# Kernel optimization log

Hardware: AMD Instinct MI355X
Metric: run time of the kernel (lower is better)

## Reference

```python
import jax, jax.numpy as jnp
import numpy as np
from jax.ops import segment_sum, segment_max

B, P, NP, EP = 128, 16, 256, 1280
EPG, ODIM, NH = 2048, 256, 128
EPS = 1e-5


def _bn(x, g, b):
    # BatchNorm1d (training-mode batch statistics), biased variance like torch
    mu = x.mean(0)
    var = ((x - mu) ** 2).mean(0)
    return g * (x - mu) * jax.lax.rsqrt(var + EPS) + b


def _gat(feat, src, dst, W, al, ar, resW, bias):
    # DGL GATConv: fc -> per-head attn logits -> leaky_relu -> edge softmax over dst -> aggregate; + residual fc + bias
    n = feat.shape[0]
    H, D = al.shape
    z = (feat @ W).reshape(n, H, D)
    el = (z * al).sum(-1)                                  # [n,H]
    er = (z * ar).sum(-1)
    e = jax.nn.leaky_relu(el[src] + er[dst], 0.2)          # [E,H]
    m = segment_max(e, dst, num_segments=n)
    ex = jnp.exp(e - m[dst])
    s = segment_sum(ex, dst, num_segments=n)
    a = ex / (s[dst] + 1e-9)
    rst = segment_sum(a[:, :, None] * z[src], dst, num_segments=n)  # [n,H,D]
    res = (feat @ resW).reshape(n, H, D)
    return (rst + res + bias.reshape(1, H, D)).reshape(n, H * D)


def _plane(feat, src, dst, p):
    # PlaneGraphEncoder forward (eval: dropout off)
    h = _gat(feat, src, dst, p['W1'], p['al1'], p['ar1'], p['res1'], p['b1'])
    h = jax.nn.relu(_bn(h, p['g1'], p['be1']))
    h = _gat(h, src, dst, p['W2'], p['al2'], p['ar2'], p['res2'], p['b2'])
    h = jax.nn.relu(_bn(h, p['g2'], p['be2']))
    rep = h.mean(0)                                        # dgl.mean_nodes -> [32]
    d = jax.nn.relu(_bn(h @ p['dW1'] + p['db1'], p['dg'], p['dbe']))
    recon = d @ p['dW2'] + p['db2']                        # [n,1]
    rloss = jnp.mean((recon - feat) ** 2)
    return rep, rloss


def _masked_gc(h, src, dst, mask_f, W, b):
    # DGL GraphConv(norm='both') with edge_weight = mask[src]*mask[dst]; structural degrees, clamp>=1
    n = h.shape[0]
    ones = jnp.ones(src.shape[0], h.dtype)
    d_out = jnp.maximum(segment_sum(ones, src, num_segments=n), 1.0)
    d_in = jnp.maximum(segment_sum(ones, dst, num_segments=n), 1.0)
    ew = mask_f[src] * mask_f[dst]                         # [E]
    hs = h * jax.lax.rsqrt(d_out)[:, None]
    agg = segment_sum(ew[:, None] * hs[src], dst, num_segments=n)
    return (agg * jax.lax.rsqrt(d_in)[:, None]) @ W + b


def _forward(plane_feat, original_features,
             W1, al1, ar1, res1, b1, g1, be1,
             W2, al2, ar2, res2, b2, g2, be2,
             dW1, db1, dg, dbe, dW2, db2,
             ft_W, ft_b, ft_g, ft_be, gc_W, gc_b, gbn_g, gbn_be,
             c1_W, c1_b, ln_g, ln_be, c2_W, c2_b,
             plane_src, plane_dst, patient_src, patient_dst, mask):
    pp = dict(W1=W1, al1=al1, ar1=ar1, res1=res1, b1=b1, g1=g1, be1=be1,
              W2=W2, al2=al2, ar2=ar2, res2=res2, b2=b2, g2=g2, be2=be2,
              dW1=dW1, db1=db1, dg=dg, dbe=dbe, dW2=dW2, db2=db2)
    enc_b = jax.vmap(_plane, in_axes=(0, 0, 0, None))      # over patients
    enc_pb = jax.vmap(enc_b, in_axes=(1, 1, 1, 0))         # over planes (params axis 0)
    reps, rlosses = enc_pb(plane_feat, plane_src, plane_dst, pp)   # [P,B,32], [P,B]
    plane_rep = jnp.transpose(reps, (1, 0, 2)).reshape(plane_feat.shape[0], -1)  # [B, P*32]
    avg_recon = rlosses.mean()                             # sum / (B*P)

    x = jnp.concatenate([original_features, plane_rep], axis=1)   # [B, fused]
    h = jax.nn.relu(_bn(x @ ft_W + ft_b, ft_g, ft_be))
    mask_f = mask.astype(h.dtype)
    h_sum = h
    for i in range(3):
        hn = _masked_gc(h, patient_src, patient_dst, mask_f, gc_W[i], gc_b[i])
        hn = jax.nn.relu(_bn(hn, gbn_g[i], gbn_be[i]))
        h = hn + h
        h_sum = h_sum + h
    h = h_sum / 4.0                                        # mean over [h0,h1,h2,h3]

    z = h @ c1_W + c1_b
    mu = z.mean(-1, keepdims=True)
    var = ((z - mu) ** 2).mean(-1, keepdims=True)
    z = jax.nn.relu(ln_g * (z - mu) * jax.lax.rsqrt(var + EPS) + ln_be)
    logits = z @ c2_W + c2_b
    return logits, avg_recon


def setup_inputs() -> dict:
    key = jax.random.key(0)
    ks = iter(jax.random.split(key, 64))
    f = lambda shape, s=0.1: jax.random.normal(next(ks), shape, jnp.float32) * s
    inp = dict(
        plane_feat=f((B, P, NP, 1), 1.0),
        plane_src=jax.random.randint(next(ks), (B, P, EP), 0, NP, jnp.int32),
        plane_dst=jax.random.randint(next(ks), (B, P, EP), 0, NP, jnp.int32),
        patient_src=jax.random.randint(next(ks), (EPG,), 0, B, jnp.int32),
        patient_dst=jax.random.randint(next(ks), (EPG,), 0, B, jnp.int32),
        original_features=f((B, ODIM), 1.0),
        mask=jax.random.randint(next(ks), (B,), 0, 2, jnp.int32),
        # per-plane encoder params, stacked over P
        W1=f((P, 1, 128)), al1=f((P, 2, 64)), ar1=f((P, 2, 64)),
        res1=f((P, 1, 128)), b1=f((P, 128)),
        g1=jnp.ones((P, 128)), be1=jnp.zeros((P, 128)),
        W2=f((P, 128, 32)), al2=f((P, 1, 32)), ar2=f((P, 1, 32)),
        res2=f((P, 128, 32)), b2=f((P, 32)),
        g2=jnp.ones((P, 32)), be2=jnp.zeros((P, 32)),
        dW1=f((P, 32, 128)), db1=f((P, 128)),
        dg=jnp.ones((P, 128)), dbe=jnp.zeros((P, 128)),
        dW2=f((P, 128, 1)), db2=f((P, 1)),
        # patient-level params
        ft_W=f((ODIM + P * 32, NH)), ft_b=f((NH,)),
        ft_g=jnp.ones((NH,)), ft_be=jnp.zeros((NH,)),
        gc_W=f((3, NH, NH)), gc_b=f((3, NH)),
        gbn_g=jnp.ones((3, NH)), gbn_be=jnp.zeros((3, NH)),
        c1_W=f((NH, NH // 2)), c1_b=f((NH // 2,)),
        ln_g=jnp.ones((NH // 2,)), ln_be=jnp.zeros((NH // 2,)),
        c2_W=f((NH // 2, 2)), c2_b=f((2,)),
    )
    return inp


def reference(plane_feat, plane_src, plane_dst, patient_src, patient_dst,
              original_features, mask,
              W1, al1, ar1, res1, b1, g1, be1,
              W2, al2, ar2, res2, b2, g2, be2,
              dW1, db1, dg, dbe, dW2, db2,
              ft_W, ft_b, ft_g, ft_be, gc_W, gc_b, gbn_g, gbn_be,
              c1_W, c1_b, ln_g, ln_be, c2_W, c2_b):
    return _forward(plane_feat, original_features,
                    W1, al1, ar1, res1, b1, g1, be1,
                    W2, al2, ar2, res2, b2, g2, be2,
                    dW1, db1, dg, dbe, dW2, db2,
                    ft_W, ft_b, ft_g, ft_be, gc_W, gc_b, gbn_g, gbn_be,
                    c1_W, c1_b, ln_g, ln_be, c2_W, c2_b,
                    plane_src, plane_dst, patient_src, patient_dst, mask)
```

## Files before the change

### kernel.cpp

```cpp
#include <hip/hip_runtime.h>

#define B_    128
#define P_    16
#define NP_   256
#define EP_   1280
#define EPG_  2048
#define ODIM_ 256
#define NH_   128

typedef __attribute__((ext_vector_type(8))) short s8_t;
typedef __attribute__((ext_vector_type(4))) short s4_t;
typedef __attribute__((ext_vector_type(4))) float f4_t;

__device__ __forceinline__ unsigned short f2b(float x) {
  unsigned u = __builtin_bit_cast(unsigned, x);
  u = (u + 0x7fffu + ((u >> 16) & 1u)) >> 16;
  return (unsigned short)u;
}
__device__ __forceinline__ float b2f(short x) {
  unsigned u = ((unsigned)(unsigned short)x) << 16;
  return __builtin_bit_cast(float, u);
}

struct SmemA {
  float f[256];
  union {
    __align__(16) unsigned short wT1[64 * 136];
    __align__(16) unsigned short z2[256 * 40];
  } u1;
  __align__(16) unsigned short dW1T[128 * 36];
  union {
    struct { float S0a[256]; float S1a[256]; } a;
    float redf[512];
  } u2;
  float el2[256], er2[256];
  union {
    struct { float abg0[128], abg1[128], abg2[128]; } a;
    struct { float al2v[32], ar2v[32], dW2v[128]; } b;
  } u3;
  union {
    int cnt[256];
    struct { float scA[32], shA[32], dscA[64], dshA[64]; } b;
  } u4;
  unsigned short esrc[1280];
  int wtot[4];
  float r8[4][8]; float stat[8]; float wA[2], wB[2];
  float rlacc;
};

__global__ __launch_bounds__(256, 3) void plane_enc(
    const float* __restrict__ feat, const int* __restrict__ esrcg, const int* __restrict__ edstg,
    const float* __restrict__ W1, const float* __restrict__ al1, const float* __restrict__ ar1,
    const float* __restrict__ res1, const float* __restrict__ b1, const float* __restrict__ g1,
    const float* __restrict__ be1,
    const float* __restrict__ W2, const float* __restrict__ al2, const float* __restrict__ ar2,
    const float* __restrict__ res2, const float* __restrict__ g2, const float* __restrict__ be2,
    const float* __restrict__ dW1, const float* __restrict__ dg, const float* __restrict__ dbe,
    const float* __restrict__ dW2, const float* __restrict__ db2,
    float* __restrict__ rep_out, float* __restrict__ rlp_out)
{
  __shared__ SmemA s;
  const int g = blockIdx.x;
  const int p = g & 15;
  const int t = threadIdx.x;
  const int lane = t & 63, wv = t >> 6;
  const int l15 = lane & 15, quad = lane >> 4;

  s.f[t] = feat[g * NP_ + t];
  if (t == 0) s.rlacc = 0.f;
  s.u4.cnt[t] = 0;
  __syncthreads();

  const int* gs = esrcg + g * EP_;
  const int* gd = edstg + g * EP_;
  for (int k = t; k < EP_; k += 256) atomicAdd(&s.u4.cnt[gd[k]], 1);
  __syncthreads();
  int v = s.u4.cnt[t];
  int incl = v;
  #pragma unroll
  for (int off = 1; off < 64; off <<= 1) {
    int n = __shfl_up(incl, off, 64);
    if (lane >= off) incl += n;
  }
  if (lane == 63) s.wtot[wv] = incl;
  __syncthreads();
  int woff = 0;
  for (int w = 0; w < wv; w++) woff += s.wtot[w];
  const int myStart = woff + incl - v;
  const int myDeg = v;
  __syncthreads();
  s.u4.cnt[t] = myStart;
  __syncthreads();
  for (int k = t; k < EP_; k += 256) {
    int d = gd[k];
    int pos = atomicAdd(&s.u4.cnt[d], 1);
    s.esrc[pos] = (unsigned short)gs[k];
  }
  {
    const float* W2g = W2 + p * 4096;
    const float* Rg  = res2 + p * 4096;
    for (int q = 0; q < 16; q++) {
      int idx = t + 256 * q;
      int k = idx >> 5, n = idx & 31;
      s.u1.wT1[n * 136 + k]        = f2b(W2g[idx]);
      s.u1.wT1[(n + 32) * 136 + k] = f2b(Rg[idx]);
    }
  }
  if (t < 128) {
    float w1v = W1[p * 128 + t];
    float a  = w1v * al1[p * 128 + t];
    float bq = w1v * ar1[p * 128 + t];
    #pragma unroll
    for (int off = 32; off > 0; off >>= 1) {
      a  += __shfl_down(a, off, 64);
      bq += __shfl_down(bq, off, 64);
    }
    if (lane == 0) { s.wA[wv] = a; s.wB[wv] = bq; }
  }
  __syncthreads();

  const float fi = s.f[t];
  float S0, S1;
  {
    const float wa0 = s.wA[0], wb0 = s.wB[0], wa1 = s.wA[1], wb1 = s.wB[1];
    float fmx = -1e30f, fmn = 1e30f;
    for (int j = 0; j < myDeg; j++) {
      float fs = s.f[s.esrc[myStart + j]];
      fmx = fmaxf(fmx, fs); fmn = fminf(fmn, fs);
    }
    float x0s = (wa0 >= 0.f) ? fmx : fmn;
    float x1s = (wa1 >= 0.f) ? fmx : fmn;
    float m0 = wa0 * x0s + wb0 * fi; m0 = m0 > 0.f ? m0 : 0.2f * m0;
    float m1 = wa1 * x1s + wb1 * fi; m1 = m1 > 0.f ? m1 : 0.2f * m1;
    float ss0 = 0.f, ss1 = 0.f, U0 = 0.f, U1 = 0.f;
    for (int j = 0; j < myDeg; j++) {
      float fs = s.f[s.esrc[myStart + j]];
      float e0 = wa0 * fs + wb0 * fi; e0 = e0 > 0.f ? e0 : 0.2f * e0;
      float e1 = wa1 * fs + wb1 * fi; e1 = e1 > 0.f ? e1 : 0.2f * e1;
      float x0 = __expf(e0 - m0), x1 = __expf(e1 - m1);
      ss0 += x0; U0 += x0 * fs;
      ss1 += x1; U1 += x1 * fs;
    }
    S0 = U0 / (ss0 + 1e-9f);
    S1 = U1 / (ss1 + 1e-9f);
    s.u2.a.S0a[t] = S0; s.u2.a.S1a[t] = S1;
  }

  {
    float vals[8] = {fi, fi * fi, S0, S0 * S0, S0 * fi, S1, S1 * S1, S1 * fi};
    #pragma unroll
    for (int d2 = 32; d2 > 0; d2 >>= 1) {
      #pragma unroll
      for (int q = 0; q < 8; q++) vals[q] += __shfl_down(vals[q], d2, 64);
    }
    if (lane == 0) {
      #pragma unroll
      for (int q = 0; q < 8; q++) s.r8[wv][q] = vals[q];
    }
  }
  __syncthreads();
  if (t < 8) s.stat[t] = (s.r8[0][t] + s.r8[1][t] + s.r8[2][t] + s.r8[3][t]) * (1.f / 256.f);
  __syncthreads();
  if (t < 128) {
    float mf = s.stat[0], ef2 = s.stat[1];
    int hh = t >> 6;
    float mS = s.stat[2 + 3 * hh], eS2 = s.stat[3 + 3 * hh], eSf = s.stat[4 + 3 * hh];
    float varS = eS2 - mS * mS, varf = ef2 - mf * mf, cov = eSf - mS * mf;
    float Wv = W1[p * 128 + t], Rv = res1[p * 128 + t], Bv = b1[p * 128 + t];
    float mu  = Wv * mS + Rv * mf + Bv;
    float var = Wv * Wv * varS + Rv * Rv * varf + 2.f * Wv * Rv * cov;
    float gn  = g1[p * 128 + t] * rsqrtf(var + 1e-5f);
    s.u3.a.abg0[t] = gn * Wv;
    s.u3.a.abg1[t] = gn * Rv;
    s.u3.a.abg2[t] = gn * (Bv - mu) + be1[p * 128 + t];
  }
  __syncthreads();

  float resv[32];
  {
    f4_t accum[4][4];
    #pragma unroll
    for (int i = 0; i < 4; i++)
      #pragma unroll
      for (int nt = 0; nt < 4; nt++) accum[i][nt] = (f4_t){0.f, 0.f, 0.f, 0.f};

    float fm[4], s0m[4], s1m[4];
    #pragma unroll
    for (int i = 0; i < 4; i++) {
      int m = (wv * 4 + i) * 16 + l15;
      fm[i] = s.f[m]; s0m[i] = s.u2.a.S0a[m]; s1m[i] = s.u2.a.S1a[m];
    }
    #pragma unroll
    for (int kt = 0; kt < 4; kt++) {
      int cbase = kt * 32 + quad * 8;
      float a0[8], a1[8], a2[8];
      #pragma unroll
      for (int j = 0; j < 8; j++) {
        a0[j] = s.u3.a.abg0[cbase + j]; a1[j] = s.u3.a.abg1[cbase + j]; a2[j] = s.u3.a.abg2[cbase + j];
      }
      s8_t afr[4];
      #pragma unroll
      for (int i = 0; i < 4; i++) {
        float Sm = (kt < 2) ? s0m[i] : s1m[i];
        union { s8_t v; unsigned short u[8]; } fu;
        #pragma unroll
        for (int j = 0; j < 8; j++) {
          float h = fmaxf(fmaf(a0[j], Sm, fmaf(a1[j], fm[i], a2[j])), 0.f);
          fu.u[j] = f2b(h);
        }
        afr[i] = fu.v;
      }
      s8_t bfr[4];
      #pragma unroll
      for (int nt = 0; nt < 4; nt++)
        bfr[nt] = *(const s8_t*)&s.u1.wT1[(nt * 16 + l15) * 136 + cbase];
      #pragma unroll
      for (int i = 0; i < 4; i++)
        #pragma unroll
        for (int nt = 0; nt < 4; nt++)
          accum[i][nt] = __builtin_amdgcn_mfma_f32_16x16x32_bf16(afr[i], bfr[nt], accum[i][nt], 0, 0, 0);
    }
    __syncthreads();
    #pragma unroll
    for (int i = 0; i < 4; i++) {
      int mBase = (wv * 4 + i) * 16 + quad * 4;
      #pragma unroll
      for (int nt = 0; nt < 2; nt++) {
        int col = nt * 16 + l15;
        #pragma unroll
        for (int r = 0; r < 4; r++)
          s.u1.z2[(mBase + r) * 40 + col] = f2b(accum[i][nt][r]);
      }
      #pragma unroll
      for (int h2 = 0; h2 < 2; h2++)
        #pragma unroll
        for (int r = 0; r < 4; r++)
          resv[(i * 2 + h2) * 4 + r] = accum[i][2 + h2][r];
    }
  }
  if (t < 32) { s.u3.b.al2v[t] = al2[p * 32 + t]; s.u3.b.ar2v[t] = ar2[p * 32 + t]; }
  if (t < 128) s.u3.b.dW2v[t] = dW2[p * 128 + t];
  {
    const float* Dg = dW1 + p * 4096;
    #pragma unroll
    for (int q = 0; q < 16; q++) {
      int idx = t + 256 * q;
      int k = idx >> 7, n = idx & 127;
      s.dW1T[n * 36 + k] = f2b(Dg[idx]);
    }
  }
  const float db2v = db2[p];
  __syncthreads();

  {
    const s8_t* zr = (const s8_t*)&s.u1.z2[t * 40];
    float el = 0.f, er = 0.f;
    #pragma unroll
    for (int q = 0; q < 4; q++) {
      s8_t vz = zr[q];
      #pragma unroll
      for (int j = 0; j < 8; j++) {
        float zv = b2f(vz[j]);
        el += zv * s.u3.b.al2v[q * 8 + j];
        er += zv * s.u3.b.ar2v[q * 8 + j];
      }
    }
    s.el2[t] = el; s.er2[t] = er;
  }
  __syncthreads();

  float hrow[32];
  {
    const float eri = s.er2[t];
    float maxel = -1e30f;
    for (int j = 0; j < myDeg; j++)
      maxel = fmaxf(maxel, s.el2[s.esrc[myStart + j]]);
    float m = maxel + eri; m = m > 0.f ? m : 0.2f * m;
    float ss = 0.f;
    #pragma unroll
    for (int d2 = 0; d2 < 32; d2++) hrow[d2] = 0.f;
    for (int j = 0; j < myDeg; j++) {
      int sj = s.esrc[myStart + j];
      float e = s.el2[sj] + eri;
      e = e > 0.f ? e : 0.2f * e;
      float x = __expf(e - m);
      ss += x;
      const s8_t* zr = (const s8_t*)&s.u1.z2[sj * 40];
      #pragma unroll
      for (int q = 0; q < 4; q++) {
        s8_t vz = zr[q];
        #pragma unroll
        for (int jj = 0; jj < 8; jj++) hrow[q * 8 + jj] += x * b2f(vz[jj]);
      }
    }
    float inv = 1.f / (ss + 1e-9f);
    #pragma unroll
    for (int d2 = 0; d2 < 32; d2++) hrow[d2] *= inv;
  }
  __syncthreads();
  #pragma unroll
  for (int i = 0; i < 4; i++) {
    int mBase = (wv * 4 + i) * 16 + quad * 4;
    #pragma unroll
    for (int h2 = 0; h2 < 2; h2++) {
      int col = h2 * 16 + l15;
      #pragma unroll
      for (int r = 0; r < 4; r++)
        s.u1.z2[(mBase + r) * 40 + col] = f2b(resv[(i * 2 + h2) * 4 + r]);
    }
  }
  __syncthreads();
  {
    const s8_t* zr = (const s8_t*)&s.u1.z2[t * 40];
    #pragma unroll
    for (int q = 0; q < 4; q++) {
      s8_t vz = zr[q];
      #pragma unroll
      for (int jj = 0; jj < 8; jj++) hrow[q * 8 + jj] += b2f(vz[jj]);
    }
  }
  #pragma unroll
  for (int d2 = 0; d2 < 32; d2++) s.u1.z2[t * 40 + d2] = f2b(hrow[d2]);
  __syncthreads();

  {
    int c = t & 31, gq = t >> 5;
    float s1 = 0.f, s2 = 0.f;
    for (int j = 0; j < 32; j++) {
      float vz = b2f((short)s.u1.z2[(gq * 32 + j) * 40 + c]);
      s1 += vz; s2 += vz * vz;
    }
    s.u2.redf[t] = s1; s.u2.redf[256 + t] = s2;
  }
  __syncthreads();
  if (t < 32) {
    float s1 = 0.f, s2 = 0.f;
    #pragma unroll
    for (int q = 0; q < 8; q++) { s1 += s.u2.redf[q * 32 + t]; s2 += s.u2.redf[256 + q * 32 + t]; }
    float mu = s1 * (1.f / 256.f);
    float var = s2 * (1.f / 256.f) - mu * mu;
    float a = g2[p * 32 + t] * rsqrtf(var + 1e-5f);
    s.u4.b.scA[t] = a; s.u4.b.shA[t] = be2[p * 32 + t] - a * mu;
  }
  __syncthreads();
  {
    int c = t & 31, gq = t >> 5;
    float a = s.u4.b.scA[c], bb = s.u4.b.shA[c];
    float s1 = 0.f;
    for (int j = 0; j < 32; j++) {
      int ad = (gq * 32 + j) * 40 + c;
      float vz = b2f((short)s.u1.z2[ad]);
      float hv = fmaxf(a * vz + bb, 0.f);
      s.u1.z2[ad] = f2b(hv);
      s1 += hv;
    }
    s.u2.redf[t] = s1;
  }
  __syncthreads();
  if (t < 32) {
    float s1 = 0.f;
    #pragma unroll
    for (int q = 0; q < 8; q++) s1 += s.u2.redf[q * 32 + t];
    rep_out[g * 32 + t] = s1 * (1.f / 256.f);
  }
  __syncthreads();

  {
    s8_t afr2[4];
    #pragma unroll
    for (int i = 0; i < 4; i++)
      afr2[i] = *(const s8_t*)&s.u1.z2[((wv * 4 + i) * 16 + l15) * 40 + quad * 8];
    float rAcc[4][4];
    #pragma unroll
    for (int i = 0; i < 4; i++)
      #pragma unroll
      for (int r = 0; r < 4; r++) rAcc[i][r] = 0.f;

    for (int half = 0; half < 2; half++) {
      __syncthreads();
      s.u2.redf[t] = 0.f; s.u2.redf[256 + t] = 0.f;
      __syncthreads();
      f4_t acc2[4][4];
      #pragma unroll
      for (int i = 0; i < 4; i++)
        #pragma unroll
        for (int nt = 0; nt < 4; nt++) acc2[i][nt] = (f4_t){0.f, 0.f, 0.f, 0.f};
      s8_t bfr[4];
      #pragma unroll
      for (int nt = 0; nt < 4; nt++) {
        const s4_t* pr = (const s4_t*)&s.dW1T[(half * 64 + nt * 16 + l15) * 36 + quad * 8];
        s4_t lo = pr[0], hi = pr[1];
        bfr[nt] = __builtin_shufflevector(lo, hi, 0, 1, 2, 3, 4, 5, 6, 7);
      }
      #pragma unroll
      for (int i = 0; i < 4; i++)
        #pragma unroll
        for (int nt = 0; nt < 4; nt++)
          acc2[i][nt] = __builtin_amdgcn_mfma_f32_16x16x32_bf16(afr2[i], bfr[nt], acc2[i][nt], 0, 0, 0);
      #pragma unroll
      for (int nt = 0; nt < 4; nt++) {
        float s1 = 0.f, s2 = 0.f;
        #pragma unroll
        for (int i = 0; i < 4; i++)
          #pragma unroll
          for (int r = 0; r < 4; r++) { float vv = acc2[i][nt][r]; s1 += vv; s2 += vv * vv; }
        atomicAdd(&s.u2.redf[nt * 16 + l15], s1);
        atomicAdd(&s.u2.redf[256 + nt * 16 + l15], s2);
      }
      __syncthreads();
      if (t < 64) {
        int col = half * 64 + t;
        float mu = s.u2.redf[t] * (1.f / 256.f);
        float var = s.u2.redf[256 + t] * (1.f / 256.f) - mu * mu;
        float a = dg[p * 128 + col] * rsqrtf(var + 1e-5f);
        s.u4.b.dscA[t] = a; s.u4.b.dshA[t] = dbe[p * 128 + col] - a * mu;
      }
      __syncthreads();
      #pragma unroll
      for (int nt = 0; nt < 4; nt++) {
        int cl = nt * 16 + l15;
        float a = s.u4.b.dscA[cl], bb = s.u4.b.dshA[cl], w2 = s.u3.b.dW2v[half * 64 + cl];
        #pragma unroll
        for (int i = 0; i < 4; i++)
          #pragma unroll
          for (int r = 0; r < 4; r++) {
            float dv = fmaxf(a * acc2[i][nt][r] + bb, 0.f);
            rAcc[i][r] += dv * w2;
          }
      }
    }
    #pragma unroll
    for (int off = 1; off < 16; off <<= 1)
      #pragma unroll
      for (int i = 0; i < 4; i++)
        #pragma unroll
        for (int r = 0; r < 4; r++) rAcc[i][r] += __shfl_xor(rAcc[i][r], off, 64);
    if (l15 == 0) {
      float sq = 0.f;
      #pragma unroll
      for (int i = 0; i < 4; i++)
        #pragma unroll
        for (int r = 0; r < 4; r++) {
          int m = (wv * 4 + i) * 16 + quad * 4 + r;
          float diff = rAcc[i][r] + db2v - s.f[m];
          sq += diff * diff;
        }
      atomicAdd(&s.rlacc, sq);
    }
  }
  __syncthreads();
  if (t == 0) rlp_out[g] = s.rlacc;
}

__global__ __launch_bounds__(256) void ft_mm(
    const float* __restrict__ orig, const float* __restrict__ rep,
    const float* __restrict__ ftW, float* __restrict__ hpre,
    const int* __restrict__ ps, const int* __restrict__ pd,
    const int* __restrict__ mask, unsigned short* __restrict__ abar,
    const float* __restrict__ gcW, unsigned short* __restrict__ gws)
{
  const int t = threadIdx.x;

  if (blockIdx.x >= 9) {
    const int layer = blockIdx.x - 9;
    const float* src = gcW + layer * 16384;
    unsigned short* dst = gws + layer * 16384;
    for (int idx = t; idx < 16384; idx += 256) dst[idx] = f2b(src[idx]);
    return;
  }

  if (blockIdx.x == 8) {
    __shared__ int aB[128 * 128];
    __shared__ int co[128], ci[128];
    __shared__ float facs[128], facd[128];
    for (int idx = t; idx < 16384; idx += 256) aB[idx] = 0;
    if (t < 128) { co[t] = 0; ci[t] = 0; }
    __syncthreads();
    for (int e = t; e < EPG_; e += 256) {
      int sN = ps[e], d = pd[e];
      atomicAdd(&co[sN], 1);
      atomicAdd(&ci[d], 1);
      atomicAdd(&aB[d * 128 + sN], 1);
    }
    __syncthreads();
    if (t < 128) {
      float mk = (float)mask[t];
      int da = co[t] > 1 ? co[t] : 1;
      int db = ci[t] > 1 ? ci[t] : 1;
      facs[t] = mk * rsqrtf((float)da);
      facd[t] = mk * rsqrtf((float)db);
    }
    __syncthreads();
    for (int idx = t; idx < 16384; idx += 256) {
      int d = idx >> 7, sN = idx & 127;
      abar[idx] = f2b((float)aB[idx] * facd[d] * facs[sN]);
    }
    return;
  }

  const int wv = t >> 6, lane = t & 63;
  const int l15 = lane & 15, quad = lane >> 4;
  const int m = blockIdx.x * 16 + l15;

  f4_t acc[2];
  acc[0] = (f4_t){0.f, 0.f, 0.f, 0.f};
  acc[1] = (f4_t){0.f, 0.f, 0.f, 0.f};
  for (int kt = 0; kt < 24; kt++) {
    int k0 = kt * 32 + quad * 8;
    const float* px = (k0 < 256) ? (orig + m * 256 + k0) : (rep + m * 512 + (k0 - 256));
    float4 xa = ((const float4*)px)[0];
    float4 xb = ((const float4*)px)[1];
    union { s8_t v; unsigned short u[8]; } fu;
    fu.u[0] = f2b(xa.x); fu.u[1] = f2b(xa.y); fu.u[2] = f2b(xa.z); fu.u[3] = f2b(xa.w);
    fu.u[4] = f2b(xb.x); fu.u[5] = f2b(xb.y); fu.u[6] = f2b(xb.z); fu.u[7] = f2b(xb.w);
    #pragma unroll
    for (int nt = 0; nt < 2; nt++) {
      int col = wv * 32 + nt * 16 + l15;
      union { s8_t v; unsigned short u[8]; } bu;
      #pragma unroll
      for (int j = 0; j < 8; j++) bu.u[j] = f2b(ftW[(k0 + j) * 128 + col]);
      acc[nt] = __builtin_amdgcn_mfma_f32_16x16x32_bf16(fu.v, bu.v, acc[nt], 0, 0, 0);
    }
  }
  #pragma unroll
  for (int nt = 0; nt < 2; nt++) {
    int col = wv * 32 + nt * 16 + l15;
    #pragma unroll
    for (int r = 0; r < 4; r++)
      hpre[(blockIdx.x * 16 + quad * 4 + r) * 128 + col] = acc[nt][r];
  }
}

struct SmemB {
  __align__(16) unsigned short arow[128 * 136];
  __align__(16) unsigned short hT[128 * 136];
  union {
    struct {
      union {
        __align__(16) unsigned short wT[128 * 136];
        float zF[128 * 68];
      } w;
      __align__(16) unsigned short aggB[128 * 136];
    } mm;
  } u;
  float redA[1024], redB[1024];
  float scB[128], shB[128];
};

__global__ __launch_bounds__(1024) void k_patient(
    const float* __restrict__ hpre, const unsigned short* __restrict__ abar,
    const float* __restrict__ ftg, const float* __restrict__ ftbe,
    const unsigned short* __restrict__ gws, const float* __restrict__ gbng,
    const float* __restrict__ gbnbe,
    const float* __restrict__ c1W, const float* __restrict__ c1b,
    const float* __restrict__ lng, const float* __restrict__ lnbe,
    const float* __restrict__ c2W, const float* __restrict__ c2b,
    const float* __restrict__ rlp, float* __restrict__ out)
{
  __shared__ SmemB s;
  const int t = threadIdx.x;
  const int w = t >> 6, lane = t & 63;
  const int l15 = lane & 15, quad = lane >> 4;
  const int mb = w & 7, nb = (w >> 3) * 64;

  for (int idx = t; idx < 16384; idx += 1024) {
    int d = idx >> 7, sN = idx & 127;
    s.arow[d * 136 + sN] = abar[idx];
  }

  f4_t acc[4];
  #pragma unroll
  for (int nt = 0; nt < 4; nt++) {
    int col = nb + nt * 16 + l15;
    #pragma unroll
    for (int r = 0; r < 4; r++)
      acc[nt][r] = hpre[(mb * 16 + quad * 4 + r) * 128 + col];
  }

  float hR[16], hsumR[16];
  {
    #pragma unroll
    for (int nt = 0; nt < 4; nt++) {
      float s1 = acc[nt][0] + acc[nt][1] + acc[nt][2] + acc[nt][3];
      float s2 = acc[nt][0]*acc[nt][0] + acc[nt][1]*acc[nt][1] + acc[nt][2]*acc[nt][2] + acc[nt][3]*acc[nt][3];
      s1 += __shfl_xor(s1, 16, 64); s1 += __shfl_xor(s1, 32, 64);
      s2 += __shfl_xor(s2, 16, 64); s2 += __shfl_xor(s2, 32, 64);
      if (quad == 0) {
        s.redA[mb * 128 + nb + nt * 16 + l15] = s1;
        s.redB[mb * 128 + nb + nt * 16 + l15] = s2;
      }
    }
    __syncthreads();
    if (t < 128) {
      float a1 = 0.f, a2 = 0.f;
      #pragma unroll
      for (int q = 0; q < 8; q++) { a1 += s.redA[q * 128 + t]; a2 += s.redB[q * 128 + t]; }
      float mu = a1 * (1.f / 128.f), var = a2 * (1.f / 128.f) - mu * mu;
      float a = ftg[t] * rsqrtf(var + 1e-5f);
      s.scB[t] = a; s.shB[t] = ftbe[t] - a * mu;
    }
    __syncthreads();
    #pragma unroll
    for (int nt = 0; nt < 4; nt++) {
      int col = nb + nt * 16 + l15;
      float a = s.scB[col], bb = s.shB[col];
      #pragma unroll
      for (int r = 0; r < 4; r++) {
        int row = mb * 16 + quad * 4 + r;
        float hv = fmaxf(a * acc[nt][r] + bb, 0.f);
        hR[nt * 4 + r] = hv; hsumR[nt * 4 + r] = hv;
        s.hT[col * 136 + row] = f2b(hv);
      }
    }
  }
  __syncthreads();

  for (int layer = 0; layer < 3; layer++) {
    #pragma unroll
    for (int q = 0; q < 16; q++) {
      int idx = t + 1024 * q;
      int kk = idx >> 7, n = idx & 127;
      s.u.mm.w.wT[n * 136 + kk] = gws[layer * 16384 + idx];
    }
    f4_t ag[4];
    #pragma unroll
    for (int nt = 0; nt < 4; nt++) ag[nt] = (f4_t){0.f, 0.f, 0.f, 0.f};
    #pragma unroll
    for (int ks = 0; ks < 4; ks++) {
      s8_t afr = *(const s8_t*)&s.arow[(mb * 16 + l15) * 136 + ks * 32 + quad * 8];
      #pragma unroll
      for (int nt = 0; nt < 4; nt++) {
        s8_t bfr = *(const s8_t*)&s.hT[(nb + nt * 16 + l15) * 136 + ks * 32 + quad * 8];
        ag[nt] = __builtin_amdgcn_mfma_f32_16x16x32_bf16(afr, bfr, ag[nt], 0, 0, 0);
      }
    }
    #pragma unroll
    for (int nt = 0; nt < 4; nt++) {
      int col = nb + nt * 16 + l15;
      #pragma unroll
      for (int r = 0; r < 4; r++)
        s.u.mm.aggB[(mb * 16 + quad * 4 + r) * 136 + col] = f2b(ag[nt][r]);
    }
    __syncthreads();
    f4_t oc[4];
    #pragma unroll
    for (int nt = 0; nt < 4; nt++) oc[nt] = (f4_t){0.f, 0.f, 0.f, 0.f};
    #pragma unroll
    for (int ks = 0; ks < 4; ks++) {
      s8_t afr = *(const s8_t*)&s.u.mm.aggB[(mb * 16 + l15) * 136 + ks * 32 + quad * 8];
      #pragma unroll
      for (int nt = 0; nt < 4; nt++) {
        s8_t bfr = *(const s8_t*)&s.u.mm.w.wT[(nb + nt * 16 + l15) * 136 + ks * 32 + quad * 8];
        oc[nt] = __builtin_amdgcn_mfma_f32_16x16x32_bf16(afr, bfr, oc[nt], 0, 0, 0);
      }
    }
    #pragma unroll
    for (int nt = 0; nt < 4; nt++) {
      float s1 = oc[nt][0] + oc[nt][1] + oc[nt][2] + oc[nt][3];
      float s2 = oc[nt][0]*oc[nt][0] + oc[nt][1]*oc[nt][1] + oc[nt][2]*oc[nt][2] + oc[nt][3]*oc[nt][3];
      s1 += __shfl_xor(s1, 16, 64); s1 += __shfl_xor(s1, 32, 64);
      s2 += __shfl_xor(s2, 16, 64); s2 += __shfl_xor(s2, 32, 64);
      if (quad == 0) {
        s.redA[mb * 128 + nb + nt * 16 + l15] = s1;
        s.redB[mb * 128 + nb + nt * 16 + l15] = s2;
      }
    }
    __syncthreads();
    if (t < 128) {
      float a1 = 0.f, a2 = 0.f;
      #pragma unroll
      for (int q = 0; q < 8; q++) { a1 += s.redA[q * 128 + t]; a2 += s.redB[q * 128 + t]; }
      float mu = a1 * (1.f / 128.f), var = a2 * (1.f / 128.f) - mu * mu;
      float a = gbng[layer * 128 + t] * rsqrtf(var + 1e-5f);
      s.scB[t] = a; s.shB[t] = gbnbe[layer * 128 + t] - a * mu;
    }
    __syncthreads();
    #pragma unroll
    for (int nt = 0; nt < 4; nt++) {
      int col = nb + nt * 16 + l15;
      float a = s.scB[col], bb = s.shB[col];
      #pragma unroll
      for (int r = 0; r < 4; r++) {
        int row = mb * 16 + quad * 4 + r;
        float hn = fmaxf(a * oc[nt][r] + bb, 0.f) + hR[nt * 4 + r];
        hR[nt * 4 + r] = hn;
        hsumR[nt * 4 + r] += hn;
        s.hT[col * 136 + row] = f2b(hn);
      }
    }
    __syncthreads();
  }

  #pragma unroll
  for (int nt = 0; nt < 4; nt++) {
    int col = nb + nt * 16 + l15;
    #pragma unroll
    for (int r = 0; r < 4; r++)
      s.u.mm.aggB[(mb * 16 + quad * 4 + r) * 136 + col] = f2b(hsumR[nt * 4 + r] * 0.25f);
  }
  #pragma unroll
  for (int q = 0; q < 8; q++) {
    int idx = t + 1024 * q;
    int n = idx & 63, kk = idx >> 6;
    s.u.mm.w.wT[n * 136 + kk] = f2b(c1W[kk * 64 + n]);
  }
  __syncthreads();
  {
    const int nb2 = (w >> 3) * 32;
    f4_t zc[2];
    #pragma unroll
    for (int nt = 0; nt < 2; nt++) zc[nt] = (f4_t){0.f, 0.f, 0.f, 0.f};
    #pragma unroll
    for (int ks = 0; ks < 4; ks++) {
      s8_t afr = *(const s8_t*)&s.u.mm.aggB[(mb * 16 + l15) * 136 + ks * 32 + quad * 8];
      #pragma unroll
      for (int nt = 0; nt < 2; nt++) {
        s8_t bfr = *(const s8_t*)&s.u.mm.w.wT[(nb2 + nt * 16 + l15) * 136 + ks * 32 + quad * 8];
        zc[nt] = __builtin_amdgcn_mfma_f32_16x16x32_bf16(afr, bfr, zc[nt], 0, 0, 0);
      }
    }
    __syncthreads();
    #pragma unroll
    for (int nt = 0; nt < 2; nt++) {
      int col = nb2 + nt * 16 + l15;
      #pragma unroll
      for (int r = 0; r < 4; r++)
        s.u.mm.w.zF[(mb * 16 + quad * 4 + r) * 68 + col] = zc[nt][r] + c1b[col];
    }
  }
  __syncthreads();
  if (t < 128) {
    float s1 = 0.f, s2 = 0.f;
    #pragma unroll
    for (int j = 0; j < 64; j++) { float zv = s.u.mm.w.zF[t * 68 + j]; s1 += zv; s2 += zv * zv; }
    float mu = s1 * (1.f / 64.f);
    float var = s2 * (1.f / 64.f) - mu * mu;
    float rs = rsqrtf(var + 1e-5f);
    float l0 = 0.f, l1 = 0.f;
    #pragma unroll
    for (int j = 0; j < 64; j++) {
      float zv = s.u.mm.w.zF[t * 68 + j];
      float zn = fmaxf(lng[j] * (zv - mu) * rs + lnbe[j], 0.f);
      l0 += zn * c2W[j * 2];
      l1 += zn * c2W[j * 2 + 1];
    }
    out[t * 2]     = l0 + c2b[0];
    out[t * 2 + 1] = l1 + c2b[1];
  }

  {
    float r = rlp[t] + rlp[t + 1024];
    #pragma unroll
    for (int off = 32; off > 0; off >>= 1) r += __shfl_down(r, off, 64);
    if (lane == 0) s.redA[w] = r;
  }
  __syncthreads();
  if (t == 0) {
    float tot = 0.f;
    #pragma unroll
    for (int i = 0; i < 16; i++) tot += s.redA[i];
    out[256] = tot * (1.f / (256.f * 2048.f));
  }
}

extern "C" void kernel_launch(void* const* d_in, const int* in_sizes, int n_in,
                              void* d_out, int out_size, void* d_ws, size_t ws_size,
                              hipStream_t stream) {
  (void)in_sizes; (void)n_in; (void)out_size; (void)ws_size;
  const float* plane_feat  = (const float*)d_in[0];
  const int*   plane_src   = (const int*)d_in[1];
  const int*   plane_dst   = (const int*)d_in[2];
  const int*   patient_src = (const int*)d_in[3];
  const int*   patient_dst = (const int*)d_in[4];
  const float* orig        = (const float*)d_in[5];
  const int*   mask        = (const int*)d_in[6];
  const float* W1   = (const float*)d_in[7];
  const float* al1  = (const float*)d_in[8];
  const float* ar1  = (const float*)d_in[9];
  const float* res1 = (const float*)d_in[10];
  const float* b1   = (const float*)d_in[11];
  const float* g1   = (const float*)d_in[12];
  const float* be1  = (const float*)d_in[13];
  const float* W2   = (const float*)d_in[14];
  const float* al2  = (const float*)d_in[15];
  const float* ar2  = (const float*)d_in[16];
  const float* res2 = (const float*)d_in[17];
  const float* g2   = (const float*)d_in[19];
  const float* be2  = (const float*)d_in[20];
  const float* dW1  = (const float*)d_in[21];
  const float* dg   = (const float*)d_in[23];
  const float* dbe  = (const float*)d_in[24];
  const float* dW2  = (const float*)d_in[25];
  const float* db2  = (const float*)d_in[26];
  const float* ftW  = (const float*)d_in[27];
  const float* ftg  = (const float*)d_in[29];
  const float* ftbe = (const float*)d_in[30];
  const float* gcW  = (const float*)d_in[31];
  const float* gbng = (const float*)d_in[33];
  const float* gbnbe= (const float*)d_in[34];
  const float* c1W  = (const float*)d_in[35];
  const float* c1b  = (const float*)d_in[36];
  const float* lng  = (const float*)d_in[37];
  const float* lnbe = (const float*)d_in[38];
  const float* c2W  = (const float*)d_in[39];
  const float* c2b  = (const float*)d_in[40];

  float* ws   = (float*)d_ws;
  float* rep  = ws;
  float* hpre = ws + 65536;
  unsigned short* abar = (unsigned short*)(ws + 81920);
  float* rlp  = ws + 90112;
  unsigned short* gws = (unsigned short*)(ws + 94208);
  float* outp = (float*)d_out;

  plane_enc<<<2048, 256, 0, stream>>>(plane_feat, plane_src, plane_dst,
      W1, al1, ar1, res1, b1, g1, be1, W2, al2, ar2, res2, g2, be2,
      dW1, dg, dbe, dW2, db2, rep, rlp);
  ft_mm<<<12, 256, 0, stream>>>(orig, rep, ftW, hpre,
      patient_src, patient_dst, mask, abar, gcW, gws);
  k_patient<<<1, 1024, 0, stream>>>(hpre, abar, ftg, ftbe,
      gws, gbng, gbnbe, c1W, c1b, lng, lnbe, c2W, c2b, rlp, outp);
}
```

Before: 316.5 us.

## Sort nodes by in-degree so wavefronts process similar-degree nodes together

Builds a per-graph degree histogram (capped at 32) and a counting-sort permutation of the nodes, then has each thread handle a degree-sorted node in both GAT aggregation loops. This targets wavefront divergence, where one high-degree node made all 64 lanes wait on the longest per-node edge loop. In exchange it adds shared-memory atomics, a serial prefix scan on thread 0, extra barriers, and scattered reads and writes through the permutation.

```diff
diff --git a/kernel.cpp b/kernel.cpp
--- a/kernel.cpp
+++ b/kernel.cpp
@@ -43,6 +43,8 @@
     struct { float scA[32], shA[32], dscA[64], dshA[64]; } b;
   } u4;
   unsigned short esrc[1280];
+  unsigned short mst[256], mdg[256], srt[256];
+  int hist[33];
   int wtot[4];
   float r8[4][8]; float stat[8]; float wA[2], wB[2];
   float rlacc;
@@ -90,7 +92,14 @@
   const int myDeg = v;
   __syncthreads();
   s.u4.cnt[t] = myStart;
-  __syncthreads();
+  s.mst[t] = (unsigned short)myStart;
+  s.mdg[t] = (unsigned short)myDeg;
+  if (t < 33) s.hist[t] = 0;
+  __syncthreads();
+  {
+    int b = myDeg < 32 ? myDeg : 32;
+    atomicAdd(&s.hist[b], 1);
+  }
   for (int k = t; k < EP_; k += 256) {
     int d = gd[k];
     int pos = atomicAdd(&s.u4.cnt[d], 1);
@@ -118,34 +127,48 @@
     if (lane == 0) { s.wA[wv] = a; s.wB[wv] = bq; }
   }
   __syncthreads();
-
-  const float fi = s.f[t];
-  float S0, S1;
-  {
+  if (t == 0) {
+    int acc = 0;
+    for (int i = 0; i < 33; i++) { int c = s.hist[i]; s.hist[i] = acc; acc += c; }
+  }
+  __syncthreads();
+  {
+    int b = myDeg < 32 ? myDeg : 32;
+    int pos = atomicAdd(&s.hist[b], 1);
+    s.srt[pos] = (unsigned short)t;
+  }
+  __syncthreads();
+
+  {
+    const int nid = s.srt[t];
+    const float fin = s.f[nid];
+    const int st2 = s.mst[nid], dg2 = s.mdg[nid];
     const float wa0 = s.wA[0], wb0 = s.wB[0], wa1 = s.wA[1], wb1 = s.wB[1];
     float fmx = -1e30f, fmn = 1e30f;
-    for (int j = 0; j < myDeg; j++) {
-      float fs = s.f[s.esrc[myStart + j]];
+    for (int j = 0; j < dg2; j++) {
+      float fs = s.f[s.esrc[st2 + j]];
       fmx = fmaxf(fmx, fs); fmn = fminf(fmn, fs);
     }
     float x0s = (wa0 >= 0.f) ? fmx : fmn;
     float x1s = (wa1 >= 0.f) ? fmx : fmn;
-    float m0 = wa0 * x0s + wb0 * fi; m0 = m0 > 0.f ? m0 : 0.2f * m0;
-    float m1 = wa1 * x1s + wb1 * fi; m1 = m1 > 0.f ? m1 : 0.2f * m1;
+    float m0 = wa0 * x0s + wb0 * fin; m0 = m0 > 0.f ? m0 : 0.2f * m0;
+    float m1 = wa1 * x1s + wb1 * fin; m1 = m1 > 0.f ? m1 : 0.2f * m1;
     float ss0 = 0.f, ss1 = 0.f, U0 = 0.f, U1 = 0.f;
-    for (int j = 0; j < myDeg; j++) {
-      float fs = s.f[s.esrc[myStart + j]];
-      float e0 = wa0 * fs + wb0 * fi; e0 = e0 > 0.f ? e0 : 0.2f * e0;
-      float e1 = wa1 * fs + wb1 * fi; e1 = e1 > 0.f ? e1 : 0.2f * e1;
+    for (int j = 0; j < dg2; j++) {
+      float fs = s.f[s.esrc[st2 + j]];
+      float e0 = wa0 * fs + wb0 * fin; e0 = e0 > 0.f ? e0 : 0.2f * e0;
+      float e1 = wa1 * fs + wb1 * fin; e1 = e1 > 0.f ? e1 : 0.2f * e1;
       float x0 = __expf(e0 - m0), x1 = __expf(e1 - m1);
       ss0 += x0; U0 += x0 * fs;
       ss1 += x1; U1 += x1 * fs;
     }
-    S0 = U0 / (ss0 + 1e-9f);
-    S1 = U1 / (ss1 + 1e-9f);
-    s.u2.a.S0a[t] = S0; s.u2.a.S1a[t] = S1;
-  }
-
+    s.u2.a.S0a[nid] = U0 / (ss0 + 1e-9f);
+    s.u2.a.S1a[nid] = U1 / (ss1 + 1e-9f);
+  }
+  __syncthreads();
+
+  const float fi = s.f[t];
+  const float S0 = s.u2.a.S0a[t], S1 = s.u2.a.S1a[t];
   {
     float vals[8] = {fi, fi * fi, S0, S0 * S0, S0 * fi, S1, S1 * S1, S1 * fi};
     #pragma unroll
@@ -270,17 +293,21 @@
   __syncthreads();
 
   float hrow[32];
-  {
-    const float eri = s.er2[t];
+  int nid2;
+  {
+    const int nid = s.srt[t];
+    nid2 = nid;
+    const float eri = s.er2[nid];
+    const int st2 = s.mst[nid], dg2 = s.mdg[nid];
     float maxel = -1e30f;
-    for (int j = 0; j < myDeg; j++)
-      maxel = fmaxf(maxel, s.el2[s.esrc[myStart + j]]);
+    for (int j = 0; j < dg2; j++)
+      maxel = fmaxf(maxel, s.el2[s.esrc[st2 + j]]);
     float m = maxel + eri; m = m > 0.f ? m : 0.2f * m;
     float ss = 0.f;
     #pragma unroll
     for (int d2 = 0; d2 < 32; d2++) hrow[d2] = 0.f;
-    for (int j = 0; j < myDeg; j++) {
-      int sj = s.esrc[myStart + j];
+    for (int j = 0; j < dg2; j++) {
+      int sj = s.esrc[st2 + j];
       float e = s.el2[sj] + eri;
       e = e > 0.f ? e : 0.2f * e;
       float x = __expf(e - m);
@@ -311,7 +338,7 @@
   }
   __syncthreads();
   {
-    const s8_t* zr = (const s8_t*)&s.u1.z2[t * 40];
+    const s8_t* zr = (const s8_t*)&s.u1.z2[nid2 * 40];
     #pragma unroll
     for (int q = 0; q < 4; q++) {
       s8_t vz = zr[q];
@@ -320,7 +347,7 @@
     }
   }
   #pragma unroll
-  for (int d2 = 0; d2 < 32; d2++) s.u1.z2[t * 40 + d2] = f2b(hrow[d2]);
+  for (int d2 = 0; d2 < 32; d2++) s.u1.z2[nid2 * 40 + d2] = f2b(hrow[d2]);
   __syncthreads();
 
   {
```

After: 317.4 us. About the same (+0.3%).
